# Kernel tuning notes

Hardware: AMD Instinct MI355X
Metric: run time of the kernel (lower is better)

## Reference

```python
import jax, jax.numpy as jnp
import numpy as np
from jax import lax

VOCAB = 32000
N_E = 1024
N_D = 1024
DEPTH = 4
L = 512
B = 8
HIGHWAY_BIAS = -3.0  # args.bias, folded into forget-gate bias


def setup_inputs() -> dict:
    key = jax.random.key(0)
    ks = jax.random.split(key, 8)
    x = jax.random.randint(ks[0], (L, B), 0, VOCAB)
    hidden = jnp.zeros((DEPTH, B, N_D), dtype=jnp.float32)
    emb = jax.random.normal(ks[1], (VOCAB, N_E), dtype=jnp.float32) * (3.0 / VOCAB) ** 0.5
    W0 = jax.random.normal(ks[2], (N_E, 4 * N_D), dtype=jnp.float32) * N_E ** -0.5
    Wl = jax.random.normal(ks[3], (DEPTH - 1, N_D, 3 * N_D), dtype=jnp.float32) * N_D ** -0.5
    vc = jax.random.normal(ks[4], (DEPTH, 2 * N_D), dtype=jnp.float32) * 0.1
    out_W = jax.random.normal(ks[5], (N_D, VOCAB), dtype=jnp.float32) * (3.0 / VOCAB) ** 0.5
    out_b = jnp.zeros((VOCAB,), dtype=jnp.float32)
    return {"x": x, "hidden": hidden, "emb": emb, "W0": W0, "Wl": Wl,
            "vc": vc, "out_W": out_W, "out_b": out_b}


def _sru_layer(u0, u1, u2, resid, vf, vr, c0):
    # u*: (L, B, d) precomputed GEMM outputs; scan only does elementwise recurrence.
    def step(c, inp):
        u0t, u1t, u2t, rt = inp
        f = jax.nn.sigmoid(u1t + vf * c + HIGHWAY_BIAS)
        r = jax.nn.sigmoid(u2t + vr * c)
        c_new = f * c + (1.0 - f) * u0t
        h = r * c_new + (1.0 - r) * rt
        return c_new, h
    c_last, hs = lax.scan(step, c0, (u0, u1, u2, resid))
    return hs, c_last


def reference(x, hidden, emb, W0, Wl, vc, out_W, out_b):
    h = emb[x]  # (L, B, n_e); dropout disabled (p=0)
    c_finals = []
    for layer in range(DEPTH):
        if layer == 0:
            U = jnp.einsum('lbe,ek->lbk', h, W0).reshape(L, B, 4, N_D)
            resid = U[:, :, 3]  # k=4: transformed input as highway residual
        else:
            U = jnp.einsum('lbd,dk->lbk', h, Wl[layer - 1]).reshape(L, B, 3, N_D)
            resid = h           # k=3: highway residual is the layer input
        vf = vc[layer, :N_D]
        vr = vc[layer, N_D:]
        h, c_last = _sru_layer(U[:, :, 0], U[:, :, 1], U[:, :, 2], resid, vf, vr, hidden[layer])
        c_finals.append(c_last)
    out = h.reshape(L * B, N_D) @ out_W + out_b  # (L*B, vocab)
    return out, jnp.stack(c_finals)
```

## Files before the change

### kernel.cpp

```cpp
#include <hip/hip_runtime.h>
#include <hip/hip_bf16.h>

#define L_SEQ 512
#define BATCH 8
#define ND 1024
#define VOCAB_N 32000
#define MROWS 4096
#define KDIM 1024
#define BK 64
#define NKT (KDIM / BK)
#define NSCAN 128

typedef unsigned short u16;
typedef unsigned int u32;
using bf16x8 = __attribute__((ext_vector_type(8))) __bf16;
using f32x4  = __attribute__((ext_vector_type(4))) float;
using u16x8  = __attribute__((ext_vector_type(8))) unsigned short;
using u16x4  = __attribute__((ext_vector_type(4))) unsigned short;

#define BAR() asm volatile("s_barrier" ::: "memory")
#define VMW(n) asm volatile("s_waitcnt vmcnt(" #n ")" ::: "memory")
#define SCHED() __builtin_amdgcn_sched_barrier(0)

static __device__ __forceinline__ u16 f2bf(float f) {
  u32 u = __builtin_bit_cast(u32, f);
  u32 r = u + 0x7FFF + ((u >> 16) & 1);
  return (u16)(r >> 16);
}
static __device__ __forceinline__ float bf2f(u16 b) {
  u32 u = ((u32)b) << 16;
  return __builtin_bit_cast(float, u);
}
static __device__ __forceinline__ void gload16(const void* g, void* l) {
  __builtin_amdgcn_global_load_lds(
      (const __attribute__((address_space(1))) void*)g,
      (__attribute__((address_space(3))) void*)l, 16, 0, 0);
}

static __device__ __forceinline__ void transpose_body(int tb, const float* __restrict__ W,
                                                      u16* __restrict__ Wt, int Ndim) {
  __shared__ float s[32][33];
  int nx = Ndim >> 5;
  int n0 = (tb % nx) * 32, k0 = (tb / nx) * 32;
  int tid = threadIdx.x;
  int tx = tid & 31, ty = tid >> 5;
#pragma unroll
  for (int i = 0; i < 4; i++)
    s[ty * 4 + i][tx] = __builtin_nontemporal_load(
        &W[(size_t)(k0 + ty * 4 + i) * Ndim + n0 + tx]);
  __syncthreads();
  int n = tid >> 3, kg = tid & 7;
  u16x4 o;
#pragma unroll
  for (int j = 0; j < 4; j++) o[j] = f2bf(s[kg * 4 + j][n]);
  *(u16x4*)(Wt + (size_t)(n0 + n) * KDIM + k0 + kg * 4) = o;
}

__global__ __launch_bounds__(256) void k_embed_t(const int* __restrict__ x,
                                                 const float* __restrict__ emb,
                                                 u16* __restrict__ h,
                                                 const float* __restrict__ Wsrc,
                                                 u16* __restrict__ WtOut, int NdimT) {
  if (blockIdx.x >= 2048) {
    transpose_body(blockIdx.x - 2048, Wsrc, WtOut, NdimT);
    return;
  }
  int t = blockIdx.x * 256 + threadIdx.x;
  int fidx = t * 8;
  int row = fidx >> 10;
  int col = fidx & 1023;
  int tok = x[row];
  const float4* src = (const float4*)(emb + (size_t)tok * ND + col);
  float4 a = src[0], b = src[1];
  u16x8 o;
  o[0]=f2bf(a.x); o[1]=f2bf(a.y); o[2]=f2bf(a.z); o[3]=f2bf(a.w);
  o[4]=f2bf(b.x); o[5]=f2bf(b.y); o[6]=f2bf(b.z); o[7]=f2bf(b.w);
  *(u16x8*)(h + fidx) = o;
}

__global__ __launch_bounds__(256) void k_transpose_cast(const float* __restrict__ W,
                                                        u16* __restrict__ Wt, int Ndim) {
  transpose_body(blockIdx.x, W, Wt, Ndim);
}

static __device__ __forceinline__ void stage_q(const u16* __restrict__ gbase,
                                               char* sm, int qdst, int w, int lane) {
  int d = (w * 64 + lane) * 16;
  int o = d ^ (((d >> 7) & 7) << 4);
  gload16(gbase + (size_t)(o >> 7) * KDIM + ((o & 127) >> 1), sm + qdst + d);
}
static __device__ __forceinline__ void stage8k(const u16* __restrict__ gbase,
                                               char* sm, int qdst, int tid) {
#pragma unroll
  for (int j = 0; j < 2; ++j) {
    int d = (j * 256 + tid) * 16;
    int o = d ^ (((d >> 7) & 7) << 4);
    gload16(gbase + (size_t)(o >> 7) * KDIM + ((o & 127) >> 1), sm + qdst + d);
  }
}

static __device__ __forceinline__ bf16x8 frag_ld(const char* sm, int base, int r, int cb) {
  int p = (r * 128 + cb) ^ ((r & 7) << 4);
  return *(const bf16x8*)(sm + base + p);
}

__global__ __launch_bounds__(512, 2) void k_gemm256(const u16* __restrict__ A,
                                                    const u16* __restrict__ Bt,
                                                    float* __restrict__ CoutF, int Ndim,
                                                    const float* __restrict__ bias) {
  extern __shared__ __align__(16) char sm[];

  int cpx = gridDim.x >> 3;
  int bid = blockIdx.x;
  int wg = (bid & 7) * cpx + (bid >> 3);
  int bm = wg & 15;
  int bn = wg >> 4;
  int m0 = bm * 256, n0 = bn * 256;

  int tid = threadIdx.x;
  int lane = tid & 63, w = tid >> 6;
  int wm = w >> 2, wn = w & 3;
  int l15 = lane & 15, hi16 = lane >> 4;
  const int rA = wm * 128 + l15, rB = wn * 64 + l15;

  f32x4 acc[8][4] = {};
  bf16x8 aA[4][2], bLo[2][2], bHi[2][2];

  const u16* Ab = A + (size_t)m0 * KDIM;
  const u16* Bb = Bt + (size_t)n0 * KDIM;

  auto stA = [&](int tile, int q) {
    stage_q(Ab + (size_t)q * 64 * KDIM + tile * 64, sm, (tile & 1) * 65536 + q * 8192, w, lane);
  };
  auto stB = [&](int tile, int q) {
    stage_q(Bb + (size_t)q * 64 * KDIM + tile * 64, sm, (tile & 1) * 65536 + 32768 + q * 8192, w, lane);
  };

#define RD_A(base, roff)                                                     \
  _Pragma("unroll") for (int kk = 0; kk < 2; ++kk)                           \
  _Pragma("unroll") for (int mi = 0; mi < 4; ++mi)                           \
      aA[mi][kk] = frag_ld(sm, (base), rA + (roff) + mi * 16, kk * 64 + hi16 * 16);
#define RD_B(dst, base, roff)                                                \
  _Pragma("unroll") for (int kk = 0; kk < 2; ++kk)                           \
  _Pragma("unroll") for (int ni = 0; ni < 2; ++ni)                           \
      dst[ni][kk] = frag_ld(sm, (base), rB + (roff) + ni * 16, kk * 64 + hi16 * 16);
#define MFMA_BLK(mOff, nOff, BREG)                                           \
  __builtin_amdgcn_s_setprio(1);                                             \
  _Pragma("unroll") for (int kk = 0; kk < 2; ++kk)                           \
  _Pragma("unroll") for (int mi = 0; mi < 4; ++mi)                           \
  _Pragma("unroll") for (int ni = 0; ni < 2; ++ni)                           \
      acc[mi + (mOff)][ni + (nOff)] = __builtin_amdgcn_mfma_f32_16x16x32_bf16( \
          aA[mi][kk], BREG[ni][kk], acc[mi + (mOff)][ni + (nOff)], 0, 0, 0); \
  __builtin_amdgcn_s_setprio(0);                                             \
  SCHED();

  stA(0, 0); stA(0, 2); stB(0, 0); stB(0, 1); stB(0, 2); stB(0, 3);
  stA(0, 1); stA(0, 3);
  stA(1, 0); stA(1, 2); stB(1, 0); stB(1, 1); stB(1, 2); stB(1, 3);
  VMW(8);
  BAR();

#pragma unroll 1
  for (int i = 0; i < 8; ++i) {
    const bool nl = (i < 7);
    const int t1 = 2 * i + 1, t2 = 2 * i + 2, t3 = 2 * i + 3;

    RD_A(0, 0); RD_B(bLo, 32768, 0);
    stA(t1, 1); stA(t1, 3);
    BAR();
    MFMA_BLK(0, 0, bLo);
    BAR();
    RD_B(bHi, 32768, 32);
    if (nl) { stA(t2, 0); stA(t2, 2); }
    BAR();
    MFMA_BLK(0, 2, bHi);
    if (nl) { VMW(10); } else { VMW(8); }
    BAR();
    RD_A(0, 64);
    if (nl) { stB(t2, 0); stB(t2, 1); }
    BAR();
    MFMA_BLK(4, 0, bLo);
    BAR();
    if (nl) { stB(t2, 2); stB(t2, 3); }
    BAR();
    MFMA_BLK(4, 2, bHi);
    if (nl) { VMW(8); } else { VMW(2); }
    BAR();

    RD_A(65536, 0); RD_B(bLo, 65536 + 32768, 0);
    if (nl) { stA(t2, 1); stA(t2, 3); }
    BAR();
    MFMA_BLK(0, 0, bLo);
    BAR();
    RD_B(bHi, 65536 + 32768, 32);
    if (nl) { stA(t3, 0); stA(t3, 2); }
    BAR();
    MFMA_BLK(0, 2, bHi);
    if (nl) { VMW(10); } else { VMW(0); }
    BAR();
    RD_A(65536, 64);
    if (nl) { stB(t3, 0); stB(t3, 1); }
    BAR();
    MFMA_BLK(4, 0, bLo);
    BAR();
    if (nl) { stB(t3, 2); stB(t3, 3); }
    BAR();
    MFMA_BLK(4, 2, bHi);
    if (nl) { VMW(8); }
    BAR();
  }
#undef RD_A
#undef RD_B
#undef MFMA_BLK

  __syncthreads();
  float* epi = (float*)sm;
  for (int p = 0; p < 4; ++p) {
    if (p) __syncthreads();
    if (wn == p) {
#pragma unroll
      for (int mi = 0; mi < 8; ++mi)
#pragma unroll
        for (int ni = 0; ni < 4; ++ni)
#pragma unroll
          for (int r = 0; r < 4; ++r)
            epi[(wm * 128 + mi * 16 + hi16 * 4 + r) * 68 + ni * 16 + l15] = acc[mi][ni][r];
    }
    __syncthreads();
    int gcolbase = n0 + p * 64;
#pragma unroll
    for (int i = 0; i < 8; ++i) {
      int fidx = i * 2048 + tid * 4;
      int row = fidx >> 6, col = fidx & 63;
      f32x4 v = *(const f32x4*)(epi + row * 68 + col);
      int gcol = gcolbase + col;
      const float4 bb = *(const float4*)(bias + gcol);
      v[0] += bb.x; v[1] += bb.y; v[2] += bb.z; v[3] += bb.w;
      __builtin_nontemporal_store(v, (f32x4*)(CoutF + (size_t)(m0 + row) * Ndim + gcol));
    }
  }
}

template <int EPI>
__global__ __launch_bounds__(256, 2) void k_gemm128(const u16* __restrict__ A,
                                                    const u16* __restrict__ Bt,
                                                    u16* __restrict__ Cout, int Ndim) {
  extern __shared__ __align__(16) char sm[];

  int cpx = gridDim.x >> 3;
  int bid = blockIdx.x;
  int wg = (bid & 7) * cpx + (bid >> 3);
  int bm = wg & 31;
  int bn = wg >> 5;
  int m0 = bm * 128, n0 = bn * 128;

  int tid = threadIdx.x;
  int lane = tid & 63, w = tid >> 6;
  int wm = w >> 1, wn = w & 1;
  int l15 = lane & 15, hi16 = lane >> 4;
  const int rA = wm * 64 + l15, rB = wn * 64 + l15;

  f32x4 acc[4][4] = {};
  bf16x8 aA[4][2], bB[4][2];

  const u16* Ab = A + (size_t)m0 * KDIM;
  const u16* Bb = Bt + (size_t)n0 * KDIM;

  auto stage_tile = [&](int t, int buf) {
    int base = buf * 32768;
    stage8k(Ab + t * 64,                     sm, base,         tid);
    stage8k(Ab + (size_t)64 * KDIM + t * 64, sm, base + 8192,  tid);
    stage8k(Bb + t * 64,                     sm, base + 16384, tid);
    stage8k(Bb + (size_t)64 * KDIM + t * 64, sm, base + 24576, tid);
  };

  stage_tile(0, 0);
  VMW(0);
  BAR();

#pragma unroll 1
  for (int t = 0; t < NKT; ++t) {
    int cur = (t & 1) * 32768;
    if (t + 1 < NKT) stage_tile(t + 1, (t & 1) ^ 1);
#pragma unroll
    for (int kk = 0; kk < 2; ++kk) {
      int cb = kk * 64 + hi16 * 16;
#pragma unroll
      for (int mi = 0; mi < 4; ++mi) aA[mi][kk] = frag_ld(sm, cur, rA + mi * 16, cb);
#pragma unroll
      for (int ni = 0; ni < 4; ++ni) bB[ni][kk] = frag_ld(sm, cur + 16384, rB + ni * 16, cb);
    }
    __builtin_amdgcn_s_setprio(1);
#pragma unroll
    for (int kk = 0; kk < 2; ++kk)
#pragma unroll
      for (int mi = 0; mi < 4; ++mi)
#pragma unroll
        for (int ni = 0; ni < 4; ++ni)
          acc[mi][ni] = __builtin_amdgcn_mfma_f32_16x16x32_bf16(aA[mi][kk], bB[ni][kk], acc[mi][ni], 0, 0, 0);
    __builtin_amdgcn_s_setprio(0);
    SCHED();
    VMW(0);
    BAR();
  }

  float* epi = (float*)sm;
  for (int p = 0; p < 2; ++p) {
    if (p) __syncthreads();
    if (wn == p) {
#pragma unroll
      for (int mi = 0; mi < 4; ++mi)
#pragma unroll
        for (int ni = 0; ni < 4; ++ni)
#pragma unroll
          for (int r = 0; r < 4; ++r)
            epi[(wm * 64 + mi * 16 + hi16 * 4 + r) * 68 + ni * 16 + l15] = acc[mi][ni][r];
    }
    __syncthreads();
    int gcolbase = n0 + p * 64;
    int plane = gcolbase >> 10;
#pragma unroll
    for (int i = 0; i < 8; ++i) {
      int fidx = i * 1024 + tid * 4;
      int row = fidx >> 6, col = fidx & 63;
      f32x4 v = *(const f32x4*)(epi + row * 68 + col);
      int gcol = gcolbase + col;
      if (plane == 1) {
#pragma unroll
        for (int j = 0; j < 4; j++) v[j] = -1.44269504f * (v[j] - 3.0f);
      } else if (plane == 2) {
#pragma unroll
        for (int j = 0; j < 4; j++) v[j] = -1.44269504f * v[j];
      }
      u16x4 o;
#pragma unroll
      for (int j = 0; j < 4; j++) o[j] = f2bf(v[j]);
      *(u16x4*)(Cout + (size_t)(m0 + row) * Ndim + gcol) = o;
    }
  }
}

__global__ __launch_bounds__(256) void k_scan(const u16* __restrict__ U, int P,
                                              const u16* __restrict__ resid, int rstride,
                                              u16* __restrict__ hout,
                                              const float* __restrict__ vc,
                                              const float* __restrict__ hidden,
                                              float* __restrict__ cfin, int layer,
                                              const float* __restrict__ Wsrc,
                                              u16* __restrict__ WtOut, int NdimT) {
  if (blockIdx.x >= NSCAN) {
    transpose_body(blockIdx.x - NSCAN, Wsrc, WtOut, NdimT);
    return;
  }
  if (threadIdx.x >= 64) return;
  int cid = blockIdx.x * 64 + threadIdx.x;
  int b = cid >> 10, d = cid & 1023;
  float vfp = -1.44269504f * vc[layer * 2048 + d];
  float vrp = -1.44269504f * vc[layer * 2048 + 1024 + d];
  float c = hidden[layer * 8192 + cid];
  const u16* pu = U + (size_t)b * P * 1024 + d;
  const u16* pr = resid + (size_t)b * rstride + d;
  u16* ph = hout + (size_t)b * 1024 + d;
  const int ustep = P * 1024;
  const int rstep = rstride;

  u16 su0[16], sa1[16], sa2[16], srs[16];
#pragma unroll
  for (int j = 0; j < 16; j++) {
    su0[j] = pu[(size_t)(8 * j) * ustep];
    sa1[j] = pu[(size_t)(8 * j) * ustep + 1024];
    sa2[j] = pu[(size_t)(8 * j) * ustep + 2048];
    srs[j] = pr[(size_t)(8 * j) * rstep];
  }
  for (int tb = 0; tb < L_SEQ; tb += 16) {
#pragma unroll
    for (int j = 0; j < 16; j++) {
      int t = tb + j;
      float u0f = bf2f(su0[j]), a1f = bf2f(sa1[j]);
      float a2f = bf2f(sa2[j]), rf = bf2f(srs[j]);
      int tp = (t + 16) & 511;
      su0[j] = pu[(size_t)(8 * tp) * ustep];
      sa1[j] = pu[(size_t)(8 * tp) * ustep + 1024];
      sa2[j] = pu[(size_t)(8 * tp) * ustep + 2048];
      srs[j] = pr[(size_t)(8 * tp) * rstep];
      float e1 = __builtin_amdgcn_exp2f(fmaf(vfp, c, a1f));
      float e2 = __builtin_amdgcn_exp2f(fmaf(vrp, c, a2f));
      float fv = __builtin_amdgcn_rcpf(1.0f + e1);
      float rv = __builtin_amdgcn_rcpf(1.0f + e2);
      float cn = fmaf(fv, c - u0f, u0f);
      float hv = fmaf(rv, cn - rf, rf);
      ph[(size_t)t * (BATCH * ND)] = f2bf(hv);
      c = cn;
    }
  }
  cfin[layer * 8192 + cid] = c;
}

extern "C" void kernel_launch(void* const* d_in, const int* in_sizes, int n_in,
                              void* d_out, int out_size, void* d_ws, size_t ws_size,
                              hipStream_t stream) {
  const int*   x      = (const int*)d_in[0];
  const float* hidden = (const float*)d_in[1];
  const float* emb    = (const float*)d_in[2];
  const float* W0     = (const float*)d_in[3];
  const float* Wl     = (const float*)d_in[4];
  const float* vc     = (const float*)d_in[5];
  const float* outW   = (const float*)d_in[6];
  const float* outb   = (const float*)d_in[7];
  float* out = (float*)d_out;

  char* ws = (char*)d_ws;
  u16* hA    = (u16*)ws;
  u16* hB    = (u16*)(ws + 8388608);
  u16* U     = (u16*)(ws + 16777216);
  u16* Wt    = (u16*)(ws + 50331648);
  float* cfin = out + (size_t)MROWS * VOCAB_N;

  const size_t wtbig_off_big = 58720256;
  bool bigws = ws_size >= (size_t)(wtbig_off_big + (size_t)VOCAB_N * KDIM * 2);
  u16* WtBig = (u16*)(ws + (bigws ? wtbig_off_big : 16777216));

  k_embed_t<<<2048 + 4096, 256, 0, stream>>>(x, emb, hA, W0, Wt, 4096);

  k_gemm128<0><<<32 * 32, 256, 65536, stream>>>(hA, Wt, U, 4096);
  k_scan<<<NSCAN + 3072, 256, 0, stream>>>(U, 4, U + 3 * 1024, 4 * 1024, hB, vc, hidden,
                                           cfin, 0, Wl, Wt, 3072);

  const u16* hin[3]  = {hB, hA, hB};
  u16*       hout[3] = {hA, hB, hA};
  for (int l = 1; l <= 3; l++) {
    k_gemm128<1><<<32 * 24, 256, 65536, stream>>>(hin[l - 1], Wt, U, 3072);
    if (l < 3) {
      k_scan<<<NSCAN + 3072, 256, 0, stream>>>(U, 3, hin[l - 1], 1024, hout[l - 1], vc,
                                               hidden, cfin, l,
                                               Wl + (size_t)l * KDIM * 3072, Wt, 3072);
    } else if (bigws) {
      k_scan<<<NSCAN + 32000, 256, 0, stream>>>(U, 3, hin[l - 1], 1024, hout[l - 1], vc,
                                                hidden, cfin, l, outW, WtBig, VOCAB_N);
    } else {
      k_scan<<<NSCAN, 256, 0, stream>>>(U, 3, hin[l - 1], 1024, hout[l - 1], vc,
                                        hidden, cfin, l, nullptr, nullptr, 32);
      k_transpose_cast<<<32000, 256, 0, stream>>>(outW, WtBig, VOCAB_N);
    }
  }

  k_gemm256<<<16 * 125, 512, 131072, stream>>>(hA, WtBig, out, VOCAB_N, outb);
}
```

Baseline: 682.4 us.

## Replace 256x256 output GEMM with simpler 128x256 triple-buffered BK=32 kernel

```diff
diff --git a/kernel.cpp b/kernel.cpp
--- a/kernel.cpp
+++ b/kernel.cpp
@@ -9,6 +9,7 @@
 #define KDIM 1024
 #define BK 64
 #define NKT (KDIM / BK)
+#define NKS 32
 #define NSCAN 128
 
 typedef unsigned short u16;
@@ -83,12 +84,6 @@
   transpose_body(blockIdx.x, W, Wt, Ndim);
 }
 
-static __device__ __forceinline__ void stage_q(const u16* __restrict__ gbase,
-                                               char* sm, int qdst, int w, int lane) {
-  int d = (w * 64 + lane) * 16;
-  int o = d ^ (((d >> 7) & 7) << 4);
-  gload16(gbase + (size_t)(o >> 7) * KDIM + ((o & 127) >> 1), sm + qdst + d);
-}
 static __device__ __forceinline__ void stage8k(const u16* __restrict__ gbase,
                                                char* sm, int qdst, int tid) {
 #pragma unroll
@@ -104,133 +99,92 @@
   return *(const bf16x8*)(sm + base + p);
 }
 
-__global__ __launch_bounds__(512, 2) void k_gemm256(const u16* __restrict__ A,
-                                                    const u16* __restrict__ Bt,
-                                                    float* __restrict__ CoutF, int Ndim,
-                                                    const float* __restrict__ bias) {
+__global__ __launch_bounds__(256, 2) void k_gemm_out(const u16* __restrict__ A,
+                                                     const u16* __restrict__ Bt,
+                                                     float* __restrict__ CoutF, int Ndim,
+                                                     const float* __restrict__ bias) {
   extern __shared__ __align__(16) char sm[];
 
   int cpx = gridDim.x >> 3;
   int bid = blockIdx.x;
   int wg = (bid & 7) * cpx + (bid >> 3);
-  int bm = wg & 15;
-  int bn = wg >> 4;
-  int m0 = bm * 256, n0 = bn * 256;
+  int bm = wg & 31;
+  int bn = wg >> 5;
+  int m0 = bm * 128, n0 = bn * 256;
 
   int tid = threadIdx.x;
   int lane = tid & 63, w = tid >> 6;
-  int wm = w >> 2, wn = w & 3;
   int l15 = lane & 15, hi16 = lane >> 4;
-  const int rA = wm * 128 + l15, rB = wn * 64 + l15;
 
   f32x4 acc[8][4] = {};
-  bf16x8 aA[4][2], bLo[2][2], bHi[2][2];
+  bf16x8 aA[8], bB[4];
 
   const u16* Ab = A + (size_t)m0 * KDIM;
   const u16* Bb = Bt + (size_t)n0 * KDIM;
 
-  auto stA = [&](int tile, int q) {
-    stage_q(Ab + (size_t)q * 64 * KDIM + tile * 64, sm, (tile & 1) * 65536 + q * 8192, w, lane);
+  auto stage = [&](int t, int base) {
+#pragma unroll
+    for (int j = 0; j < 2; ++j) {
+      int slot = j * 256 + tid;
+      gload16(Ab + (size_t)(slot >> 2) * KDIM + t * 32 + (slot & 3) * 8,
+              sm + base + slot * 16);
+    }
+#pragma unroll
+    for (int j = 0; j < 4; ++j) {
+      int slot = j * 256 + tid;
+      gload16(Bb + (size_t)(slot >> 2) * KDIM + t * 32 + (slot & 3) * 8,
+              sm + base + 8192 + slot * 16);
+    }
   };
-  auto stB = [&](int tile, int q) {
-    stage_q(Bb + (size_t)q * 64 * KDIM + tile * 64, sm, (tile & 1) * 65536 + 32768 + q * 8192, w, lane);
-  };
-
-#define RD_A(base, roff)                                                     \
-  _Pragma("unroll") for (int kk = 0; kk < 2; ++kk)                           \
-  _Pragma("unroll") for (int mi = 0; mi < 4; ++mi)                           \
-      aA[mi][kk] = frag_ld(sm, (base), rA + (roff) + mi * 16, kk * 64 + hi16 * 16);
-#define RD_B(dst, base, roff)                                                \
-  _Pragma("unroll") for (int kk = 0; kk < 2; ++kk)                           \
-  _Pragma("unroll") for (int ni = 0; ni < 2; ++ni)                           \
-      dst[ni][kk] = frag_ld(sm, (base), rB + (roff) + ni * 16, kk * 64 + hi16 * 16);
-#define MFMA_BLK(mOff, nOff, BREG)                                           \
-  __builtin_amdgcn_s_setprio(1);                                             \
-  _Pragma("unroll") for (int kk = 0; kk < 2; ++kk)                           \
-  _Pragma("unroll") for (int mi = 0; mi < 4; ++mi)                           \
-  _Pragma("unroll") for (int ni = 0; ni < 2; ++ni)                           \
-      acc[mi + (mOff)][ni + (nOff)] = __builtin_amdgcn_mfma_f32_16x16x32_bf16( \
-          aA[mi][kk], BREG[ni][kk], acc[mi + (mOff)][ni + (nOff)], 0, 0, 0); \
-  __builtin_amdgcn_s_setprio(0);                                             \
-  SCHED();
-
-  stA(0, 0); stA(0, 2); stB(0, 0); stB(0, 1); stB(0, 2); stB(0, 3);
-  stA(0, 1); stA(0, 3);
-  stA(1, 0); stA(1, 2); stB(1, 0); stB(1, 1); stB(1, 2); stB(1, 3);
-  VMW(8);
+
+  stage(0, 0);
+  stage(1, 24576);
+  VMW(6);
   BAR();
 
+  const int arow = l15 * 64 + hi16 * 16;
+  const int brow = (w * 64 + l15) * 64 + hi16 * 16;
+
+  int rb = 0, sb = 2;
 #pragma unroll 1
-  for (int i = 0; i < 8; ++i) {
-    const bool nl = (i < 7);
-    const int t1 = 2 * i + 1, t2 = 2 * i + 2, t3 = 2 * i + 3;
-
-    RD_A(0, 0); RD_B(bLo, 32768, 0);
-    stA(t1, 1); stA(t1, 3);
+  for (int t = 0; t < NKS; ++t) {
+    if (t + 2 < NKS) stage(t + 2, sb * 24576);
+    const char* cur = sm + rb * 24576;
+#pragma unroll
+    for (int mi = 0; mi < 8; ++mi) aA[mi] = *(const bf16x8*)(cur + mi * 1024 + arow);
+#pragma unroll
+    for (int ni = 0; ni < 4; ++ni) bB[ni] = *(const bf16x8*)(cur + 8192 + ni * 1024 + brow);
+    __builtin_amdgcn_s_setprio(1);
+#pragma unroll
+    for (int mi = 0; mi < 8; ++mi)
+#pragma unroll
+      for (int ni = 0; ni < 4; ++ni)
+        acc[mi][ni] = __builtin_amdgcn_mfma_f32_16x16x32_bf16(aA[mi], bB[ni], acc[mi][ni], 0, 0, 0);
+    __builtin_amdgcn_s_setprio(0);
+    SCHED();
+    if (t + 2 < NKS) { VMW(6); } else { VMW(0); }
     BAR();
-    MFMA_BLK(0, 0, bLo);
-    BAR();
-    RD_B(bHi, 32768, 32);
-    if (nl) { stA(t2, 0); stA(t2, 2); }
-    BAR();
-    MFMA_BLK(0, 2, bHi);
-    if (nl) { VMW(10); } else { VMW(8); }
-    BAR();
-    RD_A(0, 64);
-    if (nl) { stB(t2, 0); stB(t2, 1); }
-    BAR();
-    MFMA_BLK(4, 0, bLo);
-    BAR();
-    if (nl) { stB(t2, 2); stB(t2, 3); }
-    BAR();
-    MFMA_BLK(4, 2, bHi);
-    if (nl) { VMW(8); } else { VMW(2); }
-    BAR();
-
-    RD_A(65536, 0); RD_B(bLo, 65536 + 32768, 0);
-    if (nl) { stA(t2, 1); stA(t2, 3); }
-    BAR();
-    MFMA_BLK(0, 0, bLo);
-    BAR();
-    RD_B(bHi, 65536 + 32768, 32);
-    if (nl) { stA(t3, 0); stA(t3, 2); }
-    BAR();
-    MFMA_BLK(0, 2, bHi);
-    if (nl) { VMW(10); } else { VMW(0); }
-    BAR();
-    RD_A(65536, 64);
-    if (nl) { stB(t3, 0); stB(t3, 1); }
-    BAR();
-    MFMA_BLK(4, 0, bLo);
-    BAR();
-    if (nl) { stB(t3, 2); stB(t3, 3); }
-    BAR();
-    MFMA_BLK(4, 2, bHi);
-    if (nl) { VMW(8); }
-    BAR();
-  }
-#undef RD_A
-#undef RD_B
-#undef MFMA_BLK
-
-  __syncthreads();
+    rb = (rb == 2) ? 0 : rb + 1;
+    sb = (sb == 2) ? 0 : sb + 1;
+  }
+
   float* epi = (float*)sm;
   for (int p = 0; p < 4; ++p) {
     if (p) __syncthreads();
-    if (wn == p) {
+    if (w == p) {
 #pragma unroll
       for (int mi = 0; mi < 8; ++mi)
 #pragma unroll
         for (int ni = 0; ni < 4; ++ni)
 #pragma unroll
           for (int r = 0; r < 4; ++r)
-            epi[(wm * 128 + mi * 16 + hi16 * 4 + r) * 68 + ni * 16 + l15] = acc[mi][ni][r];
+            epi[(mi * 16 + hi16 * 4 + r) * 68 + ni * 16 + l15] = acc[mi][ni][r];
     }
     __syncthreads();
     int gcolbase = n0 + p * 64;
 #pragma unroll
     for (int i = 0; i < 8; ++i) {
-      int fidx = i * 2048 + tid * 4;
+      int fidx = i * 1024 + tid * 4;
       int row = fidx >> 6, col = fidx & 63;
       f32x4 v = *(const f32x4*)(epi + row * 68 + col);
       int gcol = gcolbase + col;
@@ -444,5 +398,5 @@
     }
   }
 
-  k_gemm256<<<16 * 125, 512, 131072, stream>>>(hA, WtBig, out, VOCAB_N, outb);
-}
+  k_gemm_out<<<32 * 125, 256, 73728, stream>>>(hA, WtBig, out, VOCAB_N, outb);
+}
```

Measured after the change: 689.9 us. Within noise of the previous version (+1.1%).
